# Kernel tuning notes

Hardware: AMD Instinct MI355X
Metric: run time of the kernel (lower is better)

Reference implementation:

```python
import math
import jax, jax.numpy as jnp
import numpy as np

C, H, R, PD = 256, 6, 32, 16
HEAD_SCALE = 1.0 / math.sqrt(R)


def setup_inputs() -> dict:
    key = jax.random.key(0)
    ks = jax.random.split(key, 8)
    B, Lp1 = 8, 4097
    feats = jax.random.normal(ks[0], (B, Lp1, C), dtype=jnp.float32)
    # params (stored [in, out] for x @ W)
    Wq = jax.random.normal(ks[1], (C, H * R), dtype=jnp.float32) / math.sqrt(C)
    Wk = jax.random.normal(ks[2], (C, H * R), dtype=jnp.float32) / math.sqrt(C)
    Wpi = jax.random.normal(ks[3], (C, PD), dtype=jnp.float32) / math.sqrt(C)
    bpi = jnp.zeros((PD,), jnp.float32)
    Wpj = jax.random.normal(ks[4], (C, PD), dtype=jnp.float32) / math.sqrt(C)
    bpj = jnp.zeros((PD,), jnp.float32)
    Wd = jax.random.normal(ks[5], (C, 1), dtype=jnp.float32) / math.sqrt(C)
    bd = jnp.zeros((1,), jnp.float32)
    alpha_pair = jnp.float32(0.5)
    logit_scale = jnp.float32(1.0)
    return {"feats": feats, "Wq": Wq, "Wk": Wk, "Wpi": Wpi, "bpi": bpi,
            "Wpj": Wpj, "bpj": bpj, "Wd": Wd, "bd": bd,
            "alpha_pair": alpha_pair, "logit_scale": logit_scale}


def _fold_vertices(feats):
    x = feats[:, 1:]                      # drop first token
    B, L, Cc = x.shape
    return x.reshape(B, L // 2, 2, Cc).mean(axis=2)  # [B, N, C]


def reference(feats, Wq, Wk, Wpi, bpi, Wpj, bpj, Wd, bd, alpha_pair, logit_scale):
    x = _fold_vertices(feats)             # [B, N, C]
    B, N, _ = x.shape
    Q = (x @ Wq).reshape(B, N, H, R)
    K = (x @ Wk).reshape(B, N, H, R)
    # sum over heads fused into one contraction (math-equal to per-head scores summed)
    S = jnp.einsum('bnhr,bmhr->bnm', Q, K) * HEAD_SCALE   # [B, N, N]
    a_i = jax.nn.relu(x @ Wpi + bpi)      # [B, N, PD]
    b_j = jax.nn.relu(x @ Wpj + bpj)
    S = S + jnp.maximum(alpha_pair, 0.0) * jnp.einsum('bnd,bmd->bnm', a_i, b_j)
    d = (x @ Wd + bd)[..., 0]             # [B, N]
    idx = jnp.arange(N)
    S = S.at[:, idx, idx].add(d)
    return S * jnp.maximum(logit_scale, 0.01)
```

## Files before the change

### kernel.cpp

```cpp
#include <hip/hip_runtime.h>
#include <hip/hip_bf16.h>
#include <stdint.h>

typedef __attribute__((ext_vector_type(8))) short short8;
typedef __attribute__((ext_vector_type(4))) float f32x4;

#define NB 8
#define NN 2048
#define CC 256
#define LP1 4097
#define HR 192
#define PDim 16
#define KP 256
#define NPAD 448
#define HEAD_SCALE 0.17677669529663689f

#define GLOAD16(g, l) __builtin_amdgcn_global_load_lds( \
    (const __attribute__((address_space(1))) unsigned int*)(g), \
    (__attribute__((address_space(3))) unsigned int*)(l), 16, 0, 0)

__global__ __launch_bounds__(256) void k0_prep(
    const float* __restrict__ feats,
    const float* __restrict__ Wq, const float* __restrict__ Wk,
    const float* __restrict__ Wpi, const float* __restrict__ Wpj,
    const float* __restrict__ Wd,
    __hip_bfloat16* __restrict__ xb, __hip_bfloat16* __restrict__ WT,
    unsigned* __restrict__ Ppad, unsigned* __restrict__ Rpad)
{
    const int XBN  = NB*NN*CC;
    const int WTN  = NPAD*CC;
    const int PADN = NB*NN*24;
    const int TOT  = XBN + WTN + 2*PADN;
    int stride = gridDim.x * blockDim.x;
    for (int i = blockIdx.x*blockDim.x + threadIdx.x; i < TOT; i += stride) {
        if (i < XBN) {
            int grow = i >> 8, k = i & 255;
            int b = grow >> 11, n = grow & (NN-1);
            size_t base = ((size_t)b*LP1 + 1 + 2*n)*CC + k;
            float v = 0.5f*(feats[base] + feats[base + CC]);
            xb[i] = __float2bfloat16(v);
        } else if (i < XBN + WTN) {
            int j = i - XBN;
            int c = j >> 8, k = j & 255;
            float v;
            if (c < HR)                 v = Wq[k*HR + c] * HEAD_SCALE;
            else if (c < 2*HR)          v = Wk[k*HR + (c-HR)];
            else if (c < 2*HR+PDim)     v = Wpi[k*PDim + (c-2*HR)];
            else if (c < 2*HR+2*PDim)   v = Wpj[k*PDim + (c-2*HR-PDim)];
            else if (c == 416)          v = Wd[k];
            else                        v = 0.f;
            WT[j] = __float2bfloat16(v);
        } else {
            int j = i - XBN - WTN;
            unsigned* arr = (j < PADN) ? Ppad : Rpad;
            int q = (j < PADN) ? j : j - PADN;
            int row = q / 24, cu = q % 24;
            arr[row*128 + 104 + cu] = 0u;
        }
    }
}

__global__ __launch_bounds__(256, 4) void ka_proj(
    const __hip_bfloat16* __restrict__ xb, const __hip_bfloat16* __restrict__ WT,
    const float* __restrict__ bpi, const float* __restrict__ bpj,
    const float* __restrict__ bd, const float* __restrict__ alpha_pair,
    __hip_bfloat16* __restrict__ P, __hip_bfloat16* __restrict__ R,
    float* __restrict__ dvec)
{
    int t = threadIdx.x;
    int lane = t & 63;
    int w = t >> 6;
    int l15 = lane & 15, lg = lane >> 4;
    int row0 = blockIdx.x * 32;

    const __hip_bfloat16* pA[2];
    const __hip_bfloat16* pB[7];
#pragma unroll
    for (int mi = 0; mi < 2; ++mi)
        pA[mi] = xb + (size_t)(row0 + mi*16 + l15)*KP + lg*8;
#pragma unroll
    for (int ni = 0; ni < 7; ++ni)
        pB[ni] = WT + (size_t)(w*112 + ni*16 + l15)*KP + lg*8;

    f32x4 acc[2][7];
#pragma unroll
    for (int mi = 0; mi < 2; ++mi)
#pragma unroll
        for (int ni = 0; ni < 7; ++ni)
            acc[mi][ni] = (f32x4){0.f, 0.f, 0.f, 0.f};

#pragma unroll
    for (int kk = 0; kk < 8; ++kk) {
        short8 a[2], bb[7];
#pragma unroll
        for (int mi = 0; mi < 2; ++mi) a[mi] = *(const short8*)(pA[mi] + kk*32);
#pragma unroll
        for (int ni = 0; ni < 7; ++ni) bb[ni] = *(const short8*)(pB[ni] + kk*32);
#pragma unroll
        for (int mi = 0; mi < 2; ++mi)
#pragma unroll
            for (int ni = 0; ni < 7; ++ni)
                acc[mi][ni] = __builtin_amdgcn_mfma_f32_16x16x32_bf16(
                    a[mi], bb[ni], acc[mi][ni], 0, 0, 0);
    }

    float alpha_eff = fmaxf(alpha_pair[0], 0.f);
    float bd0 = bd[0];
#pragma unroll
    for (int mi = 0; mi < 2; ++mi) {
#pragma unroll
        for (int ni = 0; ni < 7; ++ni) {
            int c = w*112 + ni*16 + l15;
#pragma unroll
            for (int j = 0; j < 4; ++j) {
                int r = mi*16 + lg*4 + j;
                int grow = row0 + r;
                int b = grow >> 11, n = grow & (NN-1);
                size_t rb = ((size_t)b*NN + n)*KP;
                float v = acc[mi][ni][j];
                if (c < HR) {
                    P[rb + c] = __float2bfloat16(v);
                } else if (c < 2*HR) {
                    R[rb + (c-HR)] = __float2bfloat16(v);
                } else if (c < 2*HR+PDim) {
                    int pc = c - 2*HR;
                    P[rb + HR + pc] = __float2bfloat16(fmaxf(v + bpi[pc], 0.f) * alpha_eff);
                } else if (c < 2*HR+2*PDim) {
                    int pc = c - 2*HR - PDim;
                    R[rb + HR + pc] = __float2bfloat16(fmaxf(v + bpj[pc], 0.f));
                } else if (c == 416) {
                    dvec[(size_t)b*NN + n] = v + bd0;
                }
            }
        }
    }
}

__global__ __launch_bounds__(256, 4) void kb_pair(
    const __hip_bfloat16* __restrict__ P, const __hip_bfloat16* __restrict__ R,
    const float* __restrict__ dvec, const float* __restrict__ logit_scale,
    float* __restrict__ out)
{
    __shared__ __hip_bfloat16 ldsA[2][128*32];
    __shared__ __hip_bfloat16 ldsB[2][128*32];

    int t = threadIdx.x;
    int lane = t & 63;
    int w = t >> 6;
    int wr = w >> 1, wc = w & 1;
    int l15 = lane & 15, lg = lane >> 4;
    int b  = blockIdx.z;
    int n0 = blockIdx.y * 128;
    int m0 = blockIdx.x * 128;

    const char* srcA[2];
    const char* srcB[2];
#pragma unroll
    for (int i = 0; i < 2; ++i) {
        int row   = i*64 + (t >> 2);
        int scolb = ((t & 3) << 4) ^ ((row & 3) << 4);
        srcA[i] = (const char*)(P + ((size_t)b*NN + n0 + row)*KP) + scolb;
        srcB[i] = (const char*)(R + ((size_t)b*NN + m0 + row)*KP) + scolb;
    }
    int ldst = w * 1024;

    int abyte = (wr*64 + l15)*64 + (((lg) ^ (l15 & 3)) << 4);
    int bbyte = (wc*64 + l15)*64 + (((lg) ^ (l15 & 3)) << 4);

    f32x4 acc[4][4];
#pragma unroll
    for (int mi = 0; mi < 4; ++mi)
#pragma unroll
        for (int ni = 0; ni < 4; ++ni)
            acc[mi][ni] = (f32x4){0.f, 0.f, 0.f, 0.f};

#pragma unroll
    for (int i = 0; i < 2; ++i) {
        GLOAD16(srcA[i], (char*)(&ldsA[0][0]) + i*4096 + ldst);
        GLOAD16(srcB[i], (char*)(&ldsB[0][0]) + i*4096 + ldst);
    }

    int buf = 0;
#pragma unroll
    for (int s = 0; s < 8; ++s) {
        __syncthreads();
        if (s < 7) {
            size_t kof = (size_t)(s + 1) * 64;
#pragma unroll
            for (int i = 0; i < 2; ++i) {
                GLOAD16(srcA[i] + kof, (char*)(&ldsA[buf ^ 1][0]) + i*4096 + ldst);
                GLOAD16(srcB[i] + kof, (char*)(&ldsB[buf ^ 1][0]) + i*4096 + ldst);
            }
        }
        short8 a[4], bb[4];
#pragma unroll
        for (int mi = 0; mi < 4; ++mi)
            a[mi] = *(const short8*)((const char*)(&ldsA[buf][0]) + abyte + mi*1024);
#pragma unroll
        for (int ni = 0; ni < 4; ++ni)
            bb[ni] = *(const short8*)((const char*)(&ldsB[buf][0]) + bbyte + ni*1024);
#pragma unroll
        for (int mi = 0; mi < 4; ++mi)
#pragma unroll
            for (int ni = 0; ni < 4; ++ni)
                acc[mi][ni] = __builtin_amdgcn_mfma_f32_16x16x32_bf16(
                    a[mi], bb[ni], acc[mi][ni], 0, 0, 0);
        buf ^= 1;
    }

    float ls = fmaxf(logit_scale[0], 0.01f);
#pragma unroll
    for (int mi = 0; mi < 4; ++mi) {
#pragma unroll
        for (int ni = 0; ni < 4; ++ni) {
            int col = m0 + wc*64 + ni*16 + l15;
#pragma unroll
            for (int j = 0; j < 4; ++j) {
                int row = n0 + wr*64 + mi*16 + lg*4 + j;
                float v = acc[mi][ni][j];
                if (row == col) v += dvec[(size_t)b*NN + row];
                out[((size_t)b*NN + row)*NN + col] = v * ls;
            }
        }
    }
}

extern "C" void kernel_launch(void* const* d_in, const int* in_sizes, int n_in,
                              void* d_out, int out_size, void* d_ws, size_t ws_size,
                              hipStream_t stream)
{
    const float* feats = (const float*)d_in[0];
    const float* Wq    = (const float*)d_in[1];
    const float* Wk    = (const float*)d_in[2];
    const float* Wpi   = (const float*)d_in[3];
    const float* bpi   = (const float*)d_in[4];
    const float* Wpj   = (const float*)d_in[5];
    const float* bpj   = (const float*)d_in[6];
    const float* Wd    = (const float*)d_in[7];
    const float* bd    = (const float*)d_in[8];
    const float* alpha = (const float*)d_in[9];
    const float* lsc   = (const float*)d_in[10];

    char* ws = (char*)d_ws;
    __hip_bfloat16* xb = (__hip_bfloat16*)(ws);
    __hip_bfloat16* WT = (__hip_bfloat16*)(ws + 8388608);
    __hip_bfloat16* P  = (__hip_bfloat16*)(ws + 8617984);
    __hip_bfloat16* R  = (__hip_bfloat16*)(ws + 17006592);
    float*          dv = (float*)(ws + 25395200);

    k0_prep<<<2048, 256, 0, stream>>>(feats, Wq, Wk, Wpi, Wpj, Wd,
                                      xb, WT, (unsigned*)P, (unsigned*)R);
    ka_proj<<<512, 256, 0, stream>>>(xb, WT, bpi, bpj, bd, alpha, P, R, dv);
    kb_pair<<<dim3(16,16,8), 256, 0, stream>>>(P, R, dv, lsc, (float*)d_out);
}
```

Measured before the change: 79.32 us.

## Shrink pair K padding, vectorize prep, remap pair grid, use nontemporal output stores

```diff
diff --git a/kernel.cpp b/kernel.cpp
--- a/kernel.cpp
+++ b/kernel.cpp
@@ -4,6 +4,7 @@
 
 typedef __attribute__((ext_vector_type(8))) short short8;
 typedef __attribute__((ext_vector_type(4))) float f32x4;
+typedef __attribute__((ext_vector_type(4))) unsigned uint4v;
 
 #define NB 8
 #define NN 2048
@@ -11,7 +12,7 @@
 #define LP1 4097
 #define HR 192
 #define PDim 16
-#define KP 256
+#define KP 224
 #define NPAD 448
 #define HEAD_SCALE 0.17677669529663689f
 
@@ -27,20 +28,32 @@
     __hip_bfloat16* __restrict__ xb, __hip_bfloat16* __restrict__ WT,
     unsigned* __restrict__ Ppad, unsigned* __restrict__ Rpad)
 {
-    const int XBN  = NB*NN*CC;
+    const int XV   = NB*NN*CC/8;
     const int WTN  = NPAD*CC;
-    const int PADN = NB*NN*24;
-    const int TOT  = XBN + WTN + 2*PADN;
+    const int PV   = NB*NN*2;
+    const int TOT  = XV + WTN + 2*PV;
     int stride = gridDim.x * blockDim.x;
     for (int i = blockIdx.x*blockDim.x + threadIdx.x; i < TOT; i += stride) {
-        if (i < XBN) {
-            int grow = i >> 8, k = i & 255;
+        if (i < XV) {
+            int grow = i >> 5, kk = (i & 31) << 3;
             int b = grow >> 11, n = grow & (NN-1);
-            size_t base = ((size_t)b*LP1 + 1 + 2*n)*CC + k;
-            float v = 0.5f*(feats[base] + feats[base + CC]);
-            xb[i] = __float2bfloat16(v);
-        } else if (i < XBN + WTN) {
-            int j = i - XBN;
+            size_t base = ((size_t)b*LP1 + 1 + 2*n)*CC + kk;
+            float4 a0 = *(const float4*)(feats + base);
+            float4 a1 = *(const float4*)(feats + base + 4);
+            float4 c0 = *(const float4*)(feats + base + CC);
+            float4 c1 = *(const float4*)(feats + base + CC + 4);
+            __hip_bfloat16 h[8];
+            h[0] = __float2bfloat16(0.5f*(a0.x + c0.x));
+            h[1] = __float2bfloat16(0.5f*(a0.y + c0.y));
+            h[2] = __float2bfloat16(0.5f*(a0.z + c0.z));
+            h[3] = __float2bfloat16(0.5f*(a0.w + c0.w));
+            h[4] = __float2bfloat16(0.5f*(a1.x + c1.x));
+            h[5] = __float2bfloat16(0.5f*(a1.y + c1.y));
+            h[6] = __float2bfloat16(0.5f*(a1.z + c1.z));
+            h[7] = __float2bfloat16(0.5f*(a1.w + c1.w));
+            *(short8*)(xb + (size_t)grow*CC + kk) = *(const short8*)h;
+        } else if (i < XV + WTN) {
+            int j = i - XV;
             int c = j >> 8, k = j & 255;
             float v;
             if (c < HR)                 v = Wq[k*HR + c] * HEAD_SCALE;
@@ -51,11 +64,11 @@
             else                        v = 0.f;
             WT[j] = __float2bfloat16(v);
         } else {
-            int j = i - XBN - WTN;
-            unsigned* arr = (j < PADN) ? Ppad : Rpad;
-            int q = (j < PADN) ? j : j - PADN;
-            int row = q / 24, cu = q % 24;
-            arr[row*128 + 104 + cu] = 0u;
+            int j = i - XV - WTN;
+            unsigned* arr = (j < PV) ? Ppad : Rpad;
+            int q = (j < PV) ? j : j - PV;
+            int row = q >> 1, of = 104 + (q & 1)*4;
+            *(uint4v*)(arr + (size_t)row*(KP/2) + of) = (uint4v){0,0,0,0};
         }
     }
 }
@@ -77,10 +90,10 @@
     const __hip_bfloat16* pB[7];
 #pragma unroll
     for (int mi = 0; mi < 2; ++mi)
-        pA[mi] = xb + (size_t)(row0 + mi*16 + l15)*KP + lg*8;
+        pA[mi] = xb + (size_t)(row0 + mi*16 + l15)*CC + lg*8;
 #pragma unroll
     for (int ni = 0; ni < 7; ++ni)
-        pB[ni] = WT + (size_t)(w*112 + ni*16 + l15)*KP + lg*8;
+        pB[ni] = WT + (size_t)(w*112 + ni*16 + l15)*CC + lg*8;
 
     f32x4 acc[2][7];
 #pragma unroll
@@ -149,9 +162,12 @@
     int w = t >> 6;
     int wr = w >> 1, wc = w & 1;
     int l15 = lane & 15, lg = lane >> 4;
-    int b  = blockIdx.z;
-    int n0 = blockIdx.y * 128;
-    int m0 = blockIdx.x * 128;
+
+    int hw = blockIdx.x;
+    int b = hw & 7;
+    int within = hw >> 3;
+    int m0 = (within & 15) << 7;
+    int n0 = (within >> 4) << 7;
 
     const char* srcA[2];
     const char* srcB[2];
@@ -164,8 +180,8 @@
     }
     int ldst = w * 1024;
 
-    int abyte = (wr*64 + l15)*64 + (((lg) ^ (l15 & 3)) << 4);
-    int bbyte = (wc*64 + l15)*64 + (((lg) ^ (l15 & 3)) << 4);
+    int abyte = (wr*64 + l15)*64 + ((lg ^ (l15 & 3)) << 4);
+    int bbyte = (wc*64 + l15)*64 + ((lg ^ (l15 & 3)) << 4);
 
     f32x4 acc[4][4];
 #pragma unroll
@@ -182,9 +198,9 @@
 
     int buf = 0;
 #pragma unroll
-    for (int s = 0; s < 8; ++s) {
+    for (int s = 0; s < 7; ++s) {
         __syncthreads();
-        if (s < 7) {
+        if (s < 6) {
             size_t kof = (size_t)(s + 1) * 64;
 #pragma unroll
             for (int i = 0; i < 2; ++i) {
@@ -219,7 +235,8 @@
                 int row = n0 + wr*64 + mi*16 + lg*4 + j;
                 float v = acc[mi][ni][j];
                 if (row == col) v += dvec[(size_t)b*NN + row];
-                out[((size_t)b*NN + row)*NN + col] = v * ls;
+                __builtin_nontemporal_store(v * ls,
+                    &out[((size_t)b*NN + row)*NN + col]);
             }
         }
     }
@@ -245,11 +262,11 @@
     __hip_bfloat16* xb = (__hip_bfloat16*)(ws);
     __hip_bfloat16* WT = (__hip_bfloat16*)(ws + 8388608);
     __hip_bfloat16* P  = (__hip_bfloat16*)(ws + 8617984);
-    __hip_bfloat16* R  = (__hip_bfloat16*)(ws + 17006592);
-    float*          dv = (float*)(ws + 25395200);
-
-    k0_prep<<<2048, 256, 0, stream>>>(feats, Wq, Wk, Wpi, Wpj, Wd,
+    __hip_bfloat16* R  = (__hip_bfloat16*)(ws + 15958016);
+    float*          dv = (float*)(ws + 23298048);
+
+    k0_prep<<<1024, 256, 0, stream>>>(feats, Wq, Wk, Wpi, Wpj, Wd,
                                       xb, WT, (unsigned*)P, (unsigned*)R);
     ka_proj<<<512, 256, 0, stream>>>(xb, WT, bpi, bpj, bd, alpha, P, R, dv);
-    kb_pair<<<dim3(16,16,8), 256, 0, stream>>>(P, R, dv, lsc, (float*)d_out);
-}
+    kb_pair<<<2048, 256, 0, stream>>>(P, R, dv, lsc, (float*)d_out);
+}
```

Measured after the change: 82.77 us. +4.3%, slower.
